# Performance work log

Hardware: AMD Instinct MI355X
Metric: run time of the kernel (lower is better)

The kernel has to match this reference:

```python
import jax, jax.numpy as jnp
import numpy as np

KS = 7       # neighborhood kernel size (fixed in __init__)
HEADS = 8    # num_heads (fixed in __init__)
LN_EPS = 1e-5


def _nbr_idx(L, k):
    # NATTEN-style clamped window: window start shifts inward at borders (no padding)
    starts = jnp.clip(jnp.arange(L) - k // 2, 0, L - k)
    idx = starts[:, None] + jnp.arange(k)            # [L, k] absolute neighbor coords
    rel = idx - jnp.arange(L)[:, None] + (k - 1)     # [L, k] rel-pos-bias index in [0, 2k-2]
    return idx, rel


def _na2d(x, qkv_w, qkv_b, proj_w, proj_b, rpb):
    # x: [B, H, W, C]  -> neighborhood attention with clamped 7x7 windows
    B, H, W, C = x.shape
    hd = C // HEADS
    qkv = x @ qkv_w.T + qkv_b                        # [B,H,W,3C]
    q, k, v = jnp.split(qkv, 3, axis=-1)
    q = q.reshape(B, H, W, HEADS, hd) * (hd ** -0.5)
    k = k.reshape(B, H, W, HEADS, hd)
    v = v.reshape(B, H, W, HEADS, hd)
    ri, rri = _nbr_idx(H, KS)                        # [H,KS]
    ci, rci = _nbr_idx(W, KS)                        # [W,KS]
    # gather neighborhoods: [B,H,W,KS,KS,heads,hd]
    kn = k[:, ri[:, None, :, None], ci[None, :, None, :]]
    vn = v[:, ri[:, None, :, None], ci[None, :, None, :]]
    scores = jnp.einsum('bijhd,bijpqhd->bhijpq', q, kn)   # [B,heads,H,W,KS,KS]
    bias = rpb[:, rri[:, None, :, None], rci[None, :, None, :]]  # [heads,H,W,KS,KS]
    scores = scores + bias[None]
    attn = jax.nn.softmax(scores.reshape(B, HEADS, H, W, KS * KS), axis=-1)
    vn = vn.reshape(B, H, W, KS * KS, HEADS, hd)
    out = jnp.einsum('bhijp,bijphd->bijhd', attn, vn)      # [B,H,W,heads,hd]
    out = out.reshape(B, H, W, C)
    return out @ proj_w.T + proj_b


def _layernorm(x, g, b):
    mu = jnp.mean(x, axis=-1, keepdims=True)
    var = jnp.mean((x - mu) ** 2, axis=-1, keepdims=True)
    return (x - mu) * jax.lax.rsqrt(var + LN_EPS) * g + b


def setup_inputs() -> dict:
    key = jax.random.key(0)
    ks = jax.random.split(key, 4)
    B, T, H, W, C = 2, 8, 48, 48, 64
    return {
        'q': jax.random.normal(ks[0], (B, T, H, W, C), dtype=jnp.float32),
        'qkv_w': jax.random.normal(ks[1], (3 * C, C), dtype=jnp.float32) * 0.02,
        'qkv_b': jnp.zeros((3 * C,), jnp.float32),
        'proj_w': jax.random.normal(ks[2], (C, C), dtype=jnp.float32) * 0.02,
        'proj_b': jnp.zeros((C,), jnp.float32),
        'rpb': jax.random.normal(ks[3], (HEADS, 2 * KS - 1, 2 * KS - 1), dtype=jnp.float32) * 0.02,
        'ln_g': jnp.ones((C,), jnp.float32),
        'ln_b': jnp.zeros((C,), jnp.float32),
    }


def reference(q, qkv_w, qkv_b, proj_w, proj_b, rpb, ln_g, ln_b):
    B, T, H, W, C = q.shape
    x = q.reshape(B * T, H, W, C)                    # '(b t) h w c'
    x = _na2d(x, qkv_w, qkv_b, proj_w, proj_b, rpb)  # wPT path
    x = x.reshape(B, T, H, W, C)
    return _layernorm(x, ln_g, ln_b)                 # norm_q; wGC=False
```

## Files before the change

### kernel.cpp

```cpp
#include <hip/hip_runtime.h>
#include <hip/hip_bf16.h>

#define BT   16
#define IH   48
#define IW   48
#define CH   64
#define NH   8
#define HD   8
#define KS   7
#define NPIX (BT*IH*IW)
#define QKVC 192
#define LN_EPS 1e-5f
#define QSCALE 0.35355339059327373f

#define TS   8
#define HS   14
#define HP   (HS*HS)
#define KVS  136
#define AOS  72

typedef __bf16 bf16_t;
typedef bf16_t bf16x8 __attribute__((ext_vector_type(8)));
typedef float  f32x4  __attribute__((ext_vector_type(4)));

__device__ __forceinline__ float bflo(unsigned u) { union { unsigned i; float f; } v; v.i = u << 16; return v.f; }
__device__ __forceinline__ float bfhi(unsigned u) { union { unsigned i; float f; } v; v.i = u & 0xffff0000u; return v.f; }

__device__ __forceinline__ void ld8bf(const __hip_bfloat16* p, float f[8]) {
    uint4 u = *reinterpret_cast<const uint4*>(p);
    f[0] = bflo(u.x); f[1] = bfhi(u.x);
    f[2] = bflo(u.y); f[3] = bfhi(u.y);
    f[4] = bflo(u.z); f[5] = bfhi(u.z);
    f[6] = bflo(u.w); f[7] = bfhi(u.w);
}

__device__ __forceinline__ bf16x8 pack_bf16x8(float4 lo, float4 hi) {
    bf16x8 r;
    r[0] = (bf16_t)lo.x; r[1] = (bf16_t)lo.y; r[2] = (bf16_t)lo.z; r[3] = (bf16_t)lo.w;
    r[4] = (bf16_t)hi.x; r[5] = (bf16_t)hi.y; r[6] = (bf16_t)hi.z; r[7] = (bf16_t)hi.w;
    return r;
}

__global__ __launch_bounds__(256) void qkv_kernel(
        const float* __restrict__ x,
        const float* __restrict__ w,
        const float* __restrict__ b,
        __hip_bfloat16* __restrict__ qkv) {
    const int gw   = blockIdx.x * 4 + (threadIdx.x >> 6);
    const int ngrp = gw % 3;
    const int mg   = gw / 3;
    const int l  = threadIdx.x & 63;
    const int m  = l & 15;
    const int kg = l >> 4;

    const int ch_base = ngrp * 64 + m * 4;
    const float4 bias4 = *(const float4*)(b + ch_base);
    const float scale = (ngrp == 0) ? QSCALE : 1.f;

    bf16x8 wb0[4], wb1[4];
    #pragma unroll
    for (int t = 0; t < 4; ++t) {
        const float* wr_ = w + (size_t)(ch_base + t) * CH + kg * 8;
        wb0[t] = pack_bf16x8(*(const float4*)(wr_),      *(const float4*)(wr_ + 4));
        wb1[t] = pack_bf16x8(*(const float4*)(wr_ + 32), *(const float4*)(wr_ + 36));
    }

    #pragma unroll
    for (int mm = 0; mm < 2; ++mm) {
        const int mtile = mg * 2 + mm;
        const float* xr = x + (size_t)(mtile * 16 + m) * CH + kg * 8;
        const bf16x8 a0 = pack_bf16x8(*(const float4*)(xr),      *(const float4*)(xr + 4));
        const bf16x8 a1 = pack_bf16x8(*(const float4*)(xr + 32), *(const float4*)(xr + 36));

        float val[4][4];
        #pragma unroll
        for (int t = 0; t < 4; ++t) {
            f32x4 acc = {0.f, 0.f, 0.f, 0.f};
            acc = __builtin_amdgcn_mfma_f32_16x16x32_bf16(a0, wb0[t], acc, 0, 0, 0);
            acc = __builtin_amdgcn_mfma_f32_16x16x32_bf16(a1, wb1[t], acc, 0, 0, 0);
            const float bias = (t == 0) ? bias4.x : (t == 1) ? bias4.y : (t == 2) ? bias4.z : bias4.w;
            #pragma unroll
            for (int r = 0; r < 4; ++r) val[t][r] = (acc[r] + bias) * scale;
        }
        #pragma unroll
        for (int r = 0; r < 4; ++r) {
            const int pix = mtile * 16 + kg * 4 + r;
            union { ushort4 u; __hip_bfloat16 hh[4]; } pk;
            #pragma unroll
            for (int t = 0; t < 4; ++t) pk.hh[t] = __float2bfloat16(val[t][r]);
            *reinterpret_cast<ushort4*>(qkv + (size_t)pix * QKVC + ch_base) = pk.u;
        }
    }
}

__global__ __launch_bounds__(512) void attn_proj_ln_kernel(
        const __hip_bfloat16* __restrict__ qkv,
        const float* __restrict__ rpb,
        const float* __restrict__ pw,
        const float* __restrict__ pb,
        const float* __restrict__ g,
        const float* __restrict__ beta,
        float* __restrict__ out) {
    __shared__ __hip_bfloat16 kv[HP * KVS];
    __shared__ __hip_bfloat16 ao[TS * TS * AOS];

    const int blk = blockIdx.x;
    const int n   = blk / 36;
    const int t2  = blk % 36;
    const int i0  = (t2 / 6) * TS;
    const int j0  = (t2 % 6) * TS;
    const int tid = threadIdx.x;

    for (int c = tid; c < HP * 16; c += 512) {
        const int px = c >> 4, part = c & 15;
        const int hr = px / HS, hc = px - hr * HS;
        int gr = i0 - 3 + hr; gr = gr < 0 ? 0 : (gr > IH - 1 ? IH - 1 : gr);
        int gc = j0 - 3 + hc; gc = gc < 0 ? 0 : (gc > IW - 1 ? IW - 1 : gc);
        const uint4 v = *reinterpret_cast<const uint4*>(
            qkv + ((size_t)(n * IH * IW + gr * IW + gc)) * QKVC + CH + part * 8);
        *reinterpret_cast<uint4*>(kv + px * KVS + part * 8) = v;
    }
    __syncthreads();

    {
        const int h  = tid & 7;
        const int pl = tid >> 3;
        const int i  = i0 + (pl >> 3);
        const int j  = j0 + (pl & 7);

        float qv[HD];
        ld8bf(qkv + ((size_t)(n * IH * IW + i * IW + j)) * QKVC + h * HD, qv);

        int si = i - 3; si = si < 0 ? 0 : (si > IH - KS ? IH - KS : si);
        int sj = j - 3; sj = sj < 0 ? 0 : (sj > IW - KS ? IW - KS : sj);
        const float* rp = rpb + h * (2*KS-1) * (2*KS-1) + (sj - j + (KS - 1));
        const int hjb = sj - (j0 - 3);

        float mrun = -1e30f, lrun = 0.f;
        float acc[HD];
        #pragma unroll
        for (int d = 0; d < HD; ++d) acc[d] = 0.f;

        for (int p = 0; p < KS; ++p) {
            const int ki = si + p;
            const float* rprow = rp + (ki - i + (KS - 1)) * (2*KS-1);
            const __hip_bfloat16* row = kv + ((ki - (i0 - 3)) * HS + hjb) * KVS + h * HD;

            float s[KS];
            #pragma unroll
            for (int qq = 0; qq < KS; ++qq) {
                float kf[HD];
                ld8bf(row + qq * KVS, kf);
                float sc = rprow[qq];
                #pragma unroll
                for (int d = 0; d < HD; ++d) sc += qv[d] * kf[d];
                s[qq] = sc;
            }
            float rm = s[0];
            #pragma unroll
            for (int qq = 1; qq < KS; ++qq) rm = fmaxf(rm, s[qq]);
            const float nm = fmaxf(mrun, rm);
            const float alpha = __expf(mrun - nm);
            mrun = nm;
            lrun *= alpha;
            #pragma unroll
            for (int d = 0; d < HD; ++d) acc[d] *= alpha;
            #pragma unroll
            for (int qq = 0; qq < KS; ++qq) {
                const float e = __expf(s[qq] - nm);
                lrun += e;
                float vf[HD];
                ld8bf(row + qq * KVS + CH, vf);
                #pragma unroll
                for (int d = 0; d < HD; ++d) acc[d] += e * vf[d];
            }
        }
        const float inv = 1.f / lrun;
        union { uint4 u; __hip_bfloat16 hh[8]; } pk;
        #pragma unroll
        for (int d = 0; d < HD; ++d) pk.hh[d] = __float2bfloat16(acc[d] * inv);
        *reinterpret_cast<uint4*>(ao + pl * AOS + h * HD) = pk.u;
    }
    __syncthreads();

    const int wv = tid >> 6;
    if (wv < 4) {
        const int l  = tid & 63;
        const int m  = l & 15;
        const int kg = l >> 4;

        const __hip_bfloat16* ar = ao + (wv * 16 + m) * AOS + kg * 8;
        const bf16x8 a0 = *reinterpret_cast<const bf16x8*>(ar);
        const bf16x8 a1 = *reinterpret_cast<const bf16x8*>(ar + 32);

        const int ch_base = m * 4;
        const float4 bias4 = *(const float4*)(pb + ch_base);

        float val[4][4];
        #pragma unroll
        for (int t = 0; t < 4; ++t) {
            const float* wr_ = pw + (size_t)(ch_base + t) * CH + kg * 8;
            const bf16x8 b0 = pack_bf16x8(*(const float4*)(wr_),      *(const float4*)(wr_ + 4));
            const bf16x8 b1 = pack_bf16x8(*(const float4*)(wr_ + 32), *(const float4*)(wr_ + 36));
            f32x4 acc = {0.f, 0.f, 0.f, 0.f};
            acc = __builtin_amdgcn_mfma_f32_16x16x32_bf16(a0, b0, acc, 0, 0, 0);
            acc = __builtin_amdgcn_mfma_f32_16x16x32_bf16(a1, b1, acc, 0, 0, 0);
            const float bias = (t == 0) ? bias4.x : (t == 1) ? bias4.y : (t == 2) ? bias4.z : bias4.w;
            #pragma unroll
            for (int r = 0; r < 4; ++r) val[t][r] = acc[r] + bias;
        }

        float sm[4];
        #pragma unroll
        for (int r = 0; r < 4; ++r) sm[r] = val[0][r] + val[1][r] + val[2][r] + val[3][r];
        #pragma unroll
        for (int mask = 1; mask <= 8; mask <<= 1) {
            #pragma unroll
            for (int r = 0; r < 4; ++r) sm[r] += __shfl_xor(sm[r], mask, 64);
        }
        float mu[4];
        #pragma unroll
        for (int r = 0; r < 4; ++r) mu[r] = sm[r] * (1.f / 64.f);

        float qs[4];
        #pragma unroll
        for (int r = 0; r < 4; ++r) {
            float a = val[0][r] - mu[r], bq = val[1][r] - mu[r];
            float c = val[2][r] - mu[r], d = val[3][r] - mu[r];
            qs[r] = a * a + bq * bq + c * c + d * d;
        }
        #pragma unroll
        for (int mask = 1; mask <= 8; mask <<= 1) {
            #pragma unroll
            for (int r = 0; r < 4; ++r) qs[r] += __shfl_xor(qs[r], mask, 64);
        }
        float rs[4];
        #pragma unroll
        for (int r = 0; r < 4; ++r) rs[r] = rsqrtf(qs[r] * (1.f / 64.f) + LN_EPS);

        const float4 g4  = *(const float4*)(g + ch_base);
        const float4 be4 = *(const float4*)(beta + ch_base);
        #pragma unroll
        for (int r = 0; r < 4; ++r) {
            const int pl = wv * 16 + kg * 4 + r;
            const int gi = i0 + (pl >> 3), gj = j0 + (pl & 7);
            float4 o;
            o.x = (val[0][r] - mu[r]) * rs[r] * g4.x + be4.x;
            o.y = (val[1][r] - mu[r]) * rs[r] * g4.y + be4.y;
            o.z = (val[2][r] - mu[r]) * rs[r] * g4.z + be4.z;
            o.w = (val[3][r] - mu[r]) * rs[r] * g4.w + be4.w;
            *reinterpret_cast<float4*>(out + ((size_t)(n * IH * IW + gi * IW + gj)) * CH + ch_base) = o;
        }
    }
}

extern "C" void kernel_launch(void* const* d_in, const int* in_sizes, int n_in,
                              void* d_out, int out_size, void* d_ws, size_t ws_size,
                              hipStream_t stream) {
    const float* x      = (const float*)d_in[0];
    const float* qkv_w  = (const float*)d_in[1];
    const float* qkv_b  = (const float*)d_in[2];
    const float* proj_w = (const float*)d_in[3];
    const float* proj_b = (const float*)d_in[4];
    const float* rpb    = (const float*)d_in[5];
    const float* ln_g   = (const float*)d_in[6];
    const float* ln_b   = (const float*)d_in[7];
    float* out = (float*)d_out;

    __hip_bfloat16* qkv = (__hip_bfloat16*)d_ws;

    qkv_kernel<<<864, 256, 0, stream>>>(x, qkv_w, qkv_b, qkv);
    attn_proj_ln_kernel<<<576, 512, 0, stream>>>(qkv, rpb, proj_w, proj_b,
                                                 ln_g, ln_b, out);
}
```

Baseline: 122.9 us.

## Fuse QKV projection into attention kernel, recomputing K/V for halo in LDS

Removes the separate QKV projection kernel and its bf16 global workspace. Each attention block now computes K and V for its 14x14 halo tile with MFMA straight into LDS, and Q for its 8x8 tile into a new LDS buffer. This drops one launch and the qkv write/read round trip through HBM. In exchange, K/V for halo pixels is recomputed by neighbouring tiles, about 3x the K/V projection work, and LDS use per block grows, which may limit occupancy.

```diff
diff --git a/kernel.cpp b/kernel.cpp
--- a/kernel.cpp
+++ b/kernel.cpp
@@ -9,15 +9,15 @@
 #define HD   8
 #define KS   7
 #define NPIX (BT*IH*IW)
-#define QKVC 192
 #define LN_EPS 1e-5f
 #define QSCALE 0.35355339059327373f
 
 #define TS   8
 #define HS   14
 #define HP   (HS*HS)
-#define KVS  136
-#define AOS  72
+#define NMT  13
+#define KVS  144
+#define AOS  80
 
 typedef __bf16 bf16_t;
 typedef bf16_t bf16x8 __attribute__((ext_vector_type(8)));
@@ -41,60 +41,10 @@
     return r;
 }
 
-__global__ __launch_bounds__(256) void qkv_kernel(
+__global__ __launch_bounds__(512, 4) void fused_kernel(
         const float* __restrict__ x,
-        const float* __restrict__ w,
-        const float* __restrict__ b,
-        __hip_bfloat16* __restrict__ qkv) {
-    const int gw   = blockIdx.x * 4 + (threadIdx.x >> 6);
-    const int ngrp = gw % 3;
-    const int mg   = gw / 3;
-    const int l  = threadIdx.x & 63;
-    const int m  = l & 15;
-    const int kg = l >> 4;
-
-    const int ch_base = ngrp * 64 + m * 4;
-    const float4 bias4 = *(const float4*)(b + ch_base);
-    const float scale = (ngrp == 0) ? QSCALE : 1.f;
-
-    bf16x8 wb0[4], wb1[4];
-    #pragma unroll
-    for (int t = 0; t < 4; ++t) {
-        const float* wr_ = w + (size_t)(ch_base + t) * CH + kg * 8;
-        wb0[t] = pack_bf16x8(*(const float4*)(wr_),      *(const float4*)(wr_ + 4));
-        wb1[t] = pack_bf16x8(*(const float4*)(wr_ + 32), *(const float4*)(wr_ + 36));
-    }
-
-    #pragma unroll
-    for (int mm = 0; mm < 2; ++mm) {
-        const int mtile = mg * 2 + mm;
-        const float* xr = x + (size_t)(mtile * 16 + m) * CH + kg * 8;
-        const bf16x8 a0 = pack_bf16x8(*(const float4*)(xr),      *(const float4*)(xr + 4));
-        const bf16x8 a1 = pack_bf16x8(*(const float4*)(xr + 32), *(const float4*)(xr + 36));
-
-        float val[4][4];
-        #pragma unroll
-        for (int t = 0; t < 4; ++t) {
-            f32x4 acc = {0.f, 0.f, 0.f, 0.f};
-            acc = __builtin_amdgcn_mfma_f32_16x16x32_bf16(a0, wb0[t], acc, 0, 0, 0);
-            acc = __builtin_amdgcn_mfma_f32_16x16x32_bf16(a1, wb1[t], acc, 0, 0, 0);
-            const float bias = (t == 0) ? bias4.x : (t == 1) ? bias4.y : (t == 2) ? bias4.z : bias4.w;
-            #pragma unroll
-            for (int r = 0; r < 4; ++r) val[t][r] = (acc[r] + bias) * scale;
-        }
-        #pragma unroll
-        for (int r = 0; r < 4; ++r) {
-            const int pix = mtile * 16 + kg * 4 + r;
-            union { ushort4 u; __hip_bfloat16 hh[4]; } pk;
-            #pragma unroll
-            for (int t = 0; t < 4; ++t) pk.hh[t] = __float2bfloat16(val[t][r]);
-            *reinterpret_cast<ushort4*>(qkv + (size_t)pix * QKVC + ch_base) = pk.u;
-        }
-    }
-}
-
-__global__ __launch_bounds__(512) void attn_proj_ln_kernel(
-        const __hip_bfloat16* __restrict__ qkv,
+        const float* __restrict__ qw,
+        const float* __restrict__ qb,
         const float* __restrict__ rpb,
         const float* __restrict__ pw,
         const float* __restrict__ pb,
@@ -102,6 +52,7 @@
         const float* __restrict__ beta,
         float* __restrict__ out) {
     __shared__ __hip_bfloat16 kv[HP * KVS];
+    __shared__ __hip_bfloat16 ql[TS * TS * AOS];
     __shared__ __hip_bfloat16 ao[TS * TS * AOS];
 
     const int blk = blockIdx.x;
@@ -110,15 +61,78 @@
     const int i0  = (t2 / 6) * TS;
     const int j0  = (t2 % 6) * TS;
     const int tid = threadIdx.x;
-
-    for (int c = tid; c < HP * 16; c += 512) {
-        const int px = c >> 4, part = c & 15;
-        const int hr = px / HS, hc = px - hr * HS;
-        int gr = i0 - 3 + hr; gr = gr < 0 ? 0 : (gr > IH - 1 ? IH - 1 : gr);
-        int gc = j0 - 3 + hc; gc = gc < 0 ? 0 : (gc > IW - 1 ? IW - 1 : gc);
-        const uint4 v = *reinterpret_cast<const uint4*>(
-            qkv + ((size_t)(n * IH * IW + gr * IW + gc)) * QKVC + CH + part * 8);
-        *reinterpret_cast<uint4*>(kv + px * KVS + part * 8) = v;
+    const int wv  = tid >> 6;
+    const int l   = tid & 63;
+    const int m   = l & 15;
+    const int kg  = l >> 4;
+    const size_t img = (size_t)n * (IH * IW);
+
+    for (int task = wv; task < 2 * NMT + 4; task += 8) {
+        const int ch4 = m * 4;
+        if (task < 2 * NMT) {
+            const int mt = task >> 1, ng = task & 1;
+            int pa = mt * 16 + m; pa = pa > HP - 1 ? HP - 1 : pa;
+            const int hr = pa / HS, hc = pa - hr * HS;
+            int gr = i0 - 3 + hr; gr = gr < 0 ? 0 : (gr > IH - 1 ? IH - 1 : gr);
+            int gc = j0 - 3 + hc; gc = gc < 0 ? 0 : (gc > IW - 1 ? IW - 1 : gc);
+            const float* xr = x + (img + gr * IW + gc) * CH + kg * 8;
+            const bf16x8 a0 = pack_bf16x8(*(const float4*)(xr),      *(const float4*)(xr + 4));
+            const bf16x8 a1 = pack_bf16x8(*(const float4*)(xr + 32), *(const float4*)(xr + 36));
+            const int wrow0 = CH + ng * CH + ch4;
+            const float4 bias4 = *(const float4*)(qb + wrow0);
+            float val[4][4];
+            #pragma unroll
+            for (int t = 0; t < 4; ++t) {
+                const float* wr_ = qw + (size_t)(wrow0 + t) * CH + kg * 8;
+                const bf16x8 b0 = pack_bf16x8(*(const float4*)(wr_),      *(const float4*)(wr_ + 4));
+                const bf16x8 b1 = pack_bf16x8(*(const float4*)(wr_ + 32), *(const float4*)(wr_ + 36));
+                f32x4 acc = {0.f, 0.f, 0.f, 0.f};
+                acc = __builtin_amdgcn_mfma_f32_16x16x32_bf16(a0, b0, acc, 0, 0, 0);
+                acc = __builtin_amdgcn_mfma_f32_16x16x32_bf16(a1, b1, acc, 0, 0, 0);
+                const float bias = (t == 0) ? bias4.x : (t == 1) ? bias4.y : (t == 2) ? bias4.z : bias4.w;
+                #pragma unroll
+                for (int r = 0; r < 4; ++r) val[t][r] = acc[r] + bias;
+            }
+            #pragma unroll
+            for (int r = 0; r < 4; ++r) {
+                const int hp = mt * 16 + kg * 4 + r;
+                if (hp < HP) {
+                    union { ushort4 u; __hip_bfloat16 hh[4]; } pk;
+                    #pragma unroll
+                    for (int t = 0; t < 4; ++t) pk.hh[t] = __float2bfloat16(val[t][r]);
+                    *reinterpret_cast<ushort4*>(kv + hp * KVS + ng * CH + ch4) = pk.u;
+                }
+            }
+        } else {
+            const int mt = task - 2 * NMT;
+            const int pa = mt * 16 + m;
+            const int gi = i0 + (pa >> 3), gj = j0 + (pa & 7);
+            const float* xr = x + (img + gi * IW + gj) * CH + kg * 8;
+            const bf16x8 a0 = pack_bf16x8(*(const float4*)(xr),      *(const float4*)(xr + 4));
+            const bf16x8 a1 = pack_bf16x8(*(const float4*)(xr + 32), *(const float4*)(xr + 36));
+            const float4 bias4 = *(const float4*)(qb + ch4);
+            float val[4][4];
+            #pragma unroll
+            for (int t = 0; t < 4; ++t) {
+                const float* wr_ = qw + (size_t)(ch4 + t) * CH + kg * 8;
+                const bf16x8 b0 = pack_bf16x8(*(const float4*)(wr_),      *(const float4*)(wr_ + 4));
+                const bf16x8 b1 = pack_bf16x8(*(const float4*)(wr_ + 32), *(const float4*)(wr_ + 36));
+                f32x4 acc = {0.f, 0.f, 0.f, 0.f};
+                acc = __builtin_amdgcn_mfma_f32_16x16x32_bf16(a0, b0, acc, 0, 0, 0);
+                acc = __builtin_amdgcn_mfma_f32_16x16x32_bf16(a1, b1, acc, 0, 0, 0);
+                const float bias = (t == 0) ? bias4.x : (t == 1) ? bias4.y : (t == 2) ? bias4.z : bias4.w;
+                #pragma unroll
+                for (int r = 0; r < 4; ++r) val[t][r] = (acc[r] + bias) * QSCALE;
+            }
+            #pragma unroll
+            for (int r = 0; r < 4; ++r) {
+                const int pl = mt * 16 + kg * 4 + r;
+                union { ushort4 u; __hip_bfloat16 hh[4]; } pk;
+                #pragma unroll
+                for (int t = 0; t < 4; ++t) pk.hh[t] = __float2bfloat16(val[t][r]);
+                *reinterpret_cast<ushort4*>(ql + pl * AOS + ch4) = pk.u;
+            }
+        }
     }
     __syncthreads();
 
@@ -129,7 +143,7 @@
         const int j  = j0 + (pl & 7);
 
         float qv[HD];
-        ld8bf(qkv + ((size_t)(n * IH * IW + i * IW + j)) * QKVC + h * HD, qv);
+        ld8bf(ql + pl * AOS + h * HD, qv);
 
         int si = i - 3; si = si < 0 ? 0 : (si > IH - KS ? IH - KS : si);
         int sj = j - 3; sj = sj < 0 ? 0 : (sj > IW - KS ? IW - KS : sj);
@@ -183,12 +197,7 @@
     }
     __syncthreads();
 
-    const int wv = tid >> 6;
     if (wv < 4) {
-        const int l  = tid & 63;
-        const int m  = l & 15;
-        const int kg = l >> 4;
-
         const __hip_bfloat16* ar = ao + (wv * 16 + m) * AOS + kg * 8;
         const bf16x8 a0 = *reinterpret_cast<const bf16x8*>(ar);
         const bf16x8 a1 = *reinterpret_cast<const bf16x8*>(ar + 32);
@@ -249,7 +258,7 @@
             o.y = (val[1][r] - mu[r]) * rs[r] * g4.y + be4.y;
             o.z = (val[2][r] - mu[r]) * rs[r] * g4.z + be4.z;
             o.w = (val[3][r] - mu[r]) * rs[r] * g4.w + be4.w;
-            *reinterpret_cast<float4*>(out + ((size_t)(n * IH * IW + gi * IW + gj)) * CH + ch_base) = o;
+            *reinterpret_cast<float4*>(out + (img + gi * IW + gj) * CH + ch_base) = o;
         }
     }
 }
@@ -267,9 +276,6 @@
     const float* ln_b   = (const float*)d_in[7];
     float* out = (float*)d_out;
 
-    __hip_bfloat16* qkv = (__hip_bfloat16*)d_ws;
-
-    qkv_kernel<<<864, 256, 0, stream>>>(x, qkv_w, qkv_b, qkv);
-    attn_proj_ln_kernel<<<576, 512, 0, stream>>>(qkv, rpb, proj_w, proj_b,
-                                                 ln_g, ln_b, out);
-}
+    fused_kernel<<<576, 512, 0, stream>>>(x, qkv_w, qkv_b, rpb,
+                                          proj_w, proj_b, ln_g, ln_b, out);
+}
```

Measured after the change: 142.7 us. 16.1% more time.
